# Kernel optimization log

Measured on AMD Instinct MI355X. Metric: run time of the kernel, lower is better.

The kernel has to match this reference:

```python
import jax, jax.numpy as jnp
import numpy as np

N = 50000      # nodes
E = 1_600_000  # edges per metapath graph
M = 3          # meta-path patterns
D = 128        # feature dim (in_size == out_size, GraphConv has no weight)
H = 128        # semantic-attention hidden size


def setup_inputs() -> dict:
    key = jax.random.key(0)
    k1, k2, k3, k4 = jax.random.split(key, 4)
    h = jax.random.normal(k1, (N, D), dtype=jnp.float32)
    # edges[m, 0] = src node ids, edges[m, 1] = dst node ids for metapath m
    edges = jax.random.randint(k2, (M, 2, E), 0, N, dtype=jnp.int32)
    W1 = jax.random.normal(k3, (D, H), dtype=jnp.float32) * 0.05
    b1 = jnp.zeros((H,), dtype=jnp.float32)
    W2 = jax.random.normal(k4, (H, 1), dtype=jnp.float32) * 0.05
    return {"h": h, "edges": edges, "W1": W1, "b1": b1, "W2": W2}


def _graph_conv_both(h, src, dst, n):
    """DGL GraphConv(norm='both', weight=None, bias=None):
    out = D_in^{-1/2} * A @ (D_out^{-1/2} * h), zero degrees clamped to 1."""
    ones = jnp.ones_like(src, dtype=h.dtype)
    out_deg = jax.ops.segment_sum(ones, src, num_segments=n)
    in_deg = jax.ops.segment_sum(ones, dst, num_segments=n)
    norm_src = jax.lax.rsqrt(jnp.maximum(out_deg, 1.0))
    norm_dst = jax.lax.rsqrt(jnp.maximum(in_deg, 1.0))
    msg = (h * norm_src[:, None])[src]                  # [E, D] gather
    agg = jax.ops.segment_sum(msg, dst, num_segments=n)  # [N, D] scatter-add
    return agg * norm_dst[:, None]


def reference(h, edges, W1, b1, W2):
    n = h.shape[0]
    m = edges.shape[0]
    # One normalized sparse aggregation per meta-path (fixed small M).
    z = jnp.stack(
        [_graph_conv_both(h, edges[i, 0], edges[i, 1], n) for i in range(m)],
        axis=1,
    )  # [N, M, D]
    # Semantic attention: project -> tanh -> score, mean over nodes, softmax over M.
    w = jnp.mean(jnp.tanh(z @ W1 + b1) @ W2, axis=0)  # [M, 1]
    beta = jax.nn.softmax(w, axis=0)                  # [M, 1]
    return jnp.sum(beta[None, :, :] * z, axis=1)      # [N, D]
```

## Files before the change

### kernel.cpp

```cpp
#include <hip/hip_runtime.h>
#include <cstdint>
#include <cstddef>

typedef unsigned int  uint;
typedef unsigned short ushort;

#define N_NODES 50000
#define N_EDGES 1600000
#define N_META  3
#define DIM     128

#define BKT       256
#define NBKT      196
#define BIN_CHUNK 16384
#define NCHUNK    98
#define CSR_CAP   10240
#define OCH       128
#define EPC       (N_EDGES / OCH)
#define OWORDS    12500
#define PREP_A    (N_META * OCH)
#define W1C_B     4

#define AT_TILE   64
#define AT_NBLK   782
#define ZSTR      72

__device__ __forceinline__ uint bf16rne(float f) {
    const uint u = __float_as_uint(f);
    return (u + 0x7FFFu + ((u >> 16) & 1u)) >> 16;
}
__device__ __forceinline__ float bflo(uint p) { return __uint_as_float(p << 16); }
__device__ __forceinline__ float bfhi(uint p) { return __uint_as_float(p & 0xFFFF0000u); }
__device__ __forceinline__ float fast_tanh(float x) {
    const float e = __expf(2.0f * x);
    return 1.0f - 2.0f / (e + 1.0f);
}

__global__ __launch_bounds__(256) void prep_kernel(
        const int* __restrict__ edges, const float* __restrict__ W1,
        int* __restrict__ bucket_cnt, uint* __restrict__ partials,
        ushort* __restrict__ W1b) {
    __shared__ __align__(16) uint sh[OWORDS];
    __shared__ uint bh[NBKT];
    const int blk = blockIdx.x;
    if (blk < PREP_A) {
        const int m = blk >> 7, c = blk & 127;
        uint4* sh4 = reinterpret_cast<uint4*>(sh);
        for (int j = threadIdx.x; j < OWORDS / 4; j += 256)
            sh4[j] = make_uint4(0u, 0u, 0u, 0u);
        for (int j = threadIdx.x; j < NBKT; j += 256) bh[j] = 0;
        __syncthreads();
        const int* src = edges + (size_t)(2 * m) * N_EDGES;
        const int* dst = edges + (size_t)(2 * m + 1) * N_EDGES;
        const int beg = c * EPC, end = beg + EPC;
        for (int i = beg + 4 * threadIdx.x; i + 4 <= end; i += 1024) {
            const uint4 s4 = *reinterpret_cast<const uint4*>(src + i);
            const uint4 d4 = *reinterpret_cast<const uint4*>(dst + i);
            atomicAdd(&sh[s4.x >> 2], 1u << (8 * (s4.x & 3)));
            atomicAdd(&sh[s4.y >> 2], 1u << (8 * (s4.y & 3)));
            atomicAdd(&sh[s4.z >> 2], 1u << (8 * (s4.z & 3)));
            atomicAdd(&sh[s4.w >> 2], 1u << (8 * (s4.w & 3)));
            atomicAdd(&bh[d4.x >> 8], 1u);
            atomicAdd(&bh[d4.y >> 8], 1u);
            atomicAdd(&bh[d4.z >> 8], 1u);
            atomicAdd(&bh[d4.w >> 8], 1u);
        }
        __syncthreads();
        uint4* outp4 = reinterpret_cast<uint4*>(
            partials + (size_t)(m * OCH + c) * OWORDS);
        for (int j = threadIdx.x; j < OWORDS / 4; j += 256) outp4[j] = sh4[j];
        for (int j = threadIdx.x; j < NBKT; j += 256)
            if (bh[j]) atomicAdd(&bucket_cnt[m * NBKT + j], (int)bh[j]);
    } else {
        const int base = (blk - PREP_A) * (DIM * DIM / W1C_B);
        for (int i = base + threadIdx.x; i < base + DIM * DIM / W1C_B; i += 256)
            W1b[i] = (ushort)bf16rne(W1[i]);
    }
}

__global__ __launch_bounds__(256) void scan_nsrc_kernel(
        const int* __restrict__ bucket_cnt, int* __restrict__ bucket_off,
        int* __restrict__ bucket_cur, int* __restrict__ row_off,
        const uint* __restrict__ partials, float* __restrict__ nsrc) {
    const int blk = blockIdx.x;
    if (blk < N_META) {
        __shared__ int sc[256];
        const int m = blk, t = threadIdx.x;
        const int v = (t < NBKT) ? bucket_cnt[m * NBKT + t] : 0;
        sc[t] = v;
        __syncthreads();
        for (int off = 1; off < 256; off <<= 1) {
            const int tt = (t >= off) ? sc[t - off] : 0;
            __syncthreads();
            sc[t] += tt;
            __syncthreads();
        }
        const int excl = sc[t] - v;
        if (t < NBKT) {
            bucket_off[m * (NBKT + 1) + t] = excl;
            bucket_cur[m * NBKT + t] = excl;
        }
        if (t == 0) {
            bucket_off[m * (NBKT + 1) + NBKT] = N_EDGES;
            row_off[m * (N_NODES + 1) + N_NODES] = N_EDGES;
        }
    } else {
        const int i = (blk - N_META) * 256 + threadIdx.x;
        if (i < N_META * N_NODES) {
            const int m = i / N_NODES, node = i - m * N_NODES;
            const int q = node >> 2, s8 = 8 * (node & 3);
            int s = 0;
#pragma unroll 8
            for (int c = 0; c < OCH; ++c)
                s += (partials[(size_t)(m * OCH + c) * OWORDS + q] >> s8) & 0xFF;
            nsrc[i] = rsqrtf(fmaxf((float)s, 1.0f));
        }
    }
}

__global__ __launch_bounds__(256) void scale_kernel(
        const float* __restrict__ h, const float* __restrict__ nsrc,
        ushort* __restrict__ hbm) {
    const int i = blockIdx.x * 256 + threadIdx.x;
    const int node = i >> 5;
    const float4 v = reinterpret_cast<const float4*>(h)[i];
    uint2* o = reinterpret_cast<uint2*>(hbm);
#pragma unroll
    for (int m = 0; m < N_META; ++m) {
        const float n = nsrc[m * N_NODES + node];
        uint2 p;
        p.x = bf16rne(v.x * n) | (bf16rne(v.y * n) << 16);
        p.y = bf16rne(v.z * n) | (bf16rne(v.w * n) << 16);
        o[(size_t)m * (N_NODES * DIM / 4) + i] = p;
    }
}

__global__ __launch_bounds__(256) void bin_kernel(
        const int* __restrict__ edges, int* __restrict__ bucket_cur,
        uint* __restrict__ pairs) {
    const int m = blockIdx.y;
    __shared__ int hist[NBKT];
    __shared__ int cur[NBKT];
    for (int j = threadIdx.x; j < NBKT; j += 256) hist[j] = 0;
    __syncthreads();
    const int* src = edges + (size_t)(2 * m) * N_EDGES;
    const int* dst = edges + (size_t)(2 * m + 1) * N_EDGES;
    const int beg = blockIdx.x * BIN_CHUNK;
    const int end = min(beg + BIN_CHUNK, N_EDGES);
    for (int i = beg + 4 * threadIdx.x; i + 4 <= end; i += 1024) {
        const uint4 d4 = *reinterpret_cast<const uint4*>(dst + i);
        atomicAdd(&hist[d4.x >> 8], 1);
        atomicAdd(&hist[d4.y >> 8], 1);
        atomicAdd(&hist[d4.z >> 8], 1);
        atomicAdd(&hist[d4.w >> 8], 1);
    }
    __syncthreads();
    for (int j = threadIdx.x; j < NBKT; j += 256) {
        const int n = hist[j];
        cur[j] = n ? atomicAdd(&bucket_cur[m * NBKT + j], n) : 0;
    }
    __syncthreads();
    uint* pm = pairs + (size_t)m * N_EDGES;
    for (int i = beg + 4 * threadIdx.x; i + 4 <= end; i += 1024) {
        const uint4 s4 = *reinterpret_cast<const uint4*>(src + i);
        const uint4 d4 = *reinterpret_cast<const uint4*>(dst + i);
        int p0 = atomicAdd(&cur[d4.x >> 8], 1);
        pm[p0] = (d4.x << 16) | s4.x;
        int p1 = atomicAdd(&cur[d4.y >> 8], 1);
        pm[p1] = (d4.y << 16) | s4.y;
        int p2 = atomicAdd(&cur[d4.z >> 8], 1);
        pm[p2] = (d4.z << 16) | s4.z;
        int p3 = atomicAdd(&cur[d4.w >> 8], 1);
        pm[p3] = (d4.w << 16) | s4.w;
    }
}

__global__ __launch_bounds__(256) void csr_kernel(
        const uint* __restrict__ pairs, const int* __restrict__ bucket_off,
        int* __restrict__ row_off, ushort* __restrict__ csr) {
    const int b = blockIdx.x, m = blockIdx.y;
    const int node_base = b * BKT;
    const int nb = min(BKT, N_NODES - node_base);
    __shared__ uint stage[CSR_CAP];
    __shared__ int hist[BKT];
    __shared__ int sc[BKT];
    __shared__ int cur[BKT];
    hist[threadIdx.x] = 0;
    __syncthreads();
    const int beg = bucket_off[m * (NBKT + 1) + b];
    const int end = bucket_off[m * (NBKT + 1) + b + 1];
    const int cnt = end - beg;
    const uint* pm = pairs + (size_t)m * N_EDGES + beg;
    for (int i = threadIdx.x; i < cnt; i += 256) {
        const uint p = pm[i];
        if (i < CSR_CAP) stage[i] = p;
        atomicAdd(&hist[(int)(p >> 16) - node_base], 1);
    }
    __syncthreads();
    const int v = hist[threadIdx.x];
    sc[threadIdx.x] = v;
    __syncthreads();
    for (int off = 1; off < BKT; off <<= 1) {
        const int t = (threadIdx.x >= off) ? sc[threadIdx.x - off] : 0;
        __syncthreads();
        sc[threadIdx.x] += t;
        __syncthreads();
    }
    const int excl = sc[threadIdx.x] - v;
    cur[threadIdx.x] = beg + excl;
    if (threadIdx.x < nb)
        row_off[m * (N_NODES + 1) + node_base + threadIdx.x] = beg + excl;
    __syncthreads();
    ushort* cm = csr + (size_t)m * N_EDGES;
    for (int i = threadIdx.x; i < cnt; i += 256) {
        const uint p = (i < CSR_CAP) ? stage[i] : pm[i];
        const int dl = (int)(p >> 16) - node_base;
        const int pos = atomicAdd(&cur[dl], 1);
        cm[pos] = (ushort)(p & 0xFFFFu);
    }
}

__global__ __launch_bounds__(256) void gather_kernel(
        const ushort* __restrict__ hbm, const ushort* __restrict__ csr,
        const int* __restrict__ row_off, ushort* __restrict__ zb) {
    const int m    = blockIdx.y;
    const int wave = threadIdx.x >> 6;
    const int lane = threadIdx.x & 63;
    const int q    = lane >> 4;
    const int c16  = lane & 15;
    const int node = blockIdx.x * 4 + wave;
    const int* ro = row_off + m * (N_NODES + 1);
    const int beg = ro[node];
    const int end = ro[node + 1];
    const ushort* srcs = csr + (size_t)m * N_EDGES;
    const ushort* tab  = hbm + (size_t)m * N_NODES * DIM;
    float acc[8] = {};
    int j = beg;
    for (; j + 16 <= end; j += 16) {
        int s[4]; uint4 hv[4];
#pragma unroll
        for (int u = 0; u < 4; ++u) s[u] = srcs[j + 4 * u + q];
#pragma unroll
        for (int u = 0; u < 4; ++u)
            hv[u] = *reinterpret_cast<const uint4*>(tab + (size_t)s[u] * DIM + c16 * 8);
#pragma unroll
        for (int u = 0; u < 4; ++u) {
            acc[0] += bflo(hv[u].x); acc[1] += bfhi(hv[u].x);
            acc[2] += bflo(hv[u].y); acc[3] += bfhi(hv[u].y);
            acc[4] += bflo(hv[u].z); acc[5] += bfhi(hv[u].z);
            acc[6] += bflo(hv[u].w); acc[7] += bfhi(hv[u].w);
        }
    }
    for (; j + 4 <= end; j += 4) {
        const int s0 = srcs[j + q];
        const uint4 hv = *reinterpret_cast<const uint4*>(tab + (size_t)s0 * DIM + c16 * 8);
        acc[0] += bflo(hv.x); acc[1] += bfhi(hv.x);
        acc[2] += bflo(hv.y); acc[3] += bfhi(hv.y);
        acc[4] += bflo(hv.z); acc[5] += bfhi(hv.z);
        acc[6] += bflo(hv.w); acc[7] += bfhi(hv.w);
    }
    if (j + q < end) {
        const int s0 = srcs[j + q];
        const uint4 hv = *reinterpret_cast<const uint4*>(tab + (size_t)s0 * DIM + c16 * 8);
        acc[0] += bflo(hv.x); acc[1] += bfhi(hv.x);
        acc[2] += bflo(hv.y); acc[3] += bfhi(hv.y);
        acc[4] += bflo(hv.z); acc[5] += bfhi(hv.z);
        acc[6] += bflo(hv.w); acc[7] += bfhi(hv.w);
    }
#pragma unroll
    for (int k = 0; k < 8; ++k) {
        acc[k] += __shfl_xor(acc[k], 16);
        acc[k] += __shfl_xor(acc[k], 32);
    }
    if (lane < 16) {
        const float nd = rsqrtf(fmaxf((float)(end - beg), 1.0f));
        uint4 o;
        o.x = bf16rne(acc[0] * nd) | (bf16rne(acc[1] * nd) << 16);
        o.y = bf16rne(acc[2] * nd) | (bf16rne(acc[3] * nd) << 16);
        o.z = bf16rne(acc[4] * nd) | (bf16rne(acc[5] * nd) << 16);
        o.w = bf16rne(acc[6] * nd) | (bf16rne(acc[7] * nd) << 16);
        *reinterpret_cast<uint4*>(
            zb + ((size_t)m * N_NODES + node) * DIM + c16 * 8) = o;
    }
}

__global__ __launch_bounds__(256) void attn_kernel(
        const ushort* __restrict__ zb, const ushort* __restrict__ W1b,
        const float* __restrict__ b1, const float* __restrict__ W2,
        float* __restrict__ wacc) {
    const int m   = blockIdx.y;
    const int tid = threadIdx.x;
    __shared__ __align__(16) ushort zT[DIM * ZSTR];
    __shared__ __align__(16) ushort w1s[DIM * DIM];
    __shared__ float red[4];

    {
        const uint4* s = reinterpret_cast<const uint4*>(W1b);
        uint4* dst = reinterpret_cast<uint4*>(w1s);
        for (int i = tid; i < DIM * DIM / 8; i += 256) dst[i] = s[i];
    }
    const int node_base = blockIdx.x * AT_TILE;
    for (int i = tid; i < AT_TILE * (DIM / 8); i += 256) {
        const int n = i >> 4, dq = i & 15;
        int row = node_base + n;
        if (row >= N_NODES) row = N_NODES - 1;
        const uint4 v = *reinterpret_cast<const uint4*>(
            zb + ((size_t)m * N_NODES + row) * DIM + dq * 8);
        ushort* cptr = &zT[(8 * dq) * ZSTR + n];
        cptr[0 * ZSTR] = (ushort)(v.x & 0xFFFFu); cptr[1 * ZSTR] = (ushort)(v.x >> 16);
        cptr[2 * ZSTR] = (ushort)(v.y & 0xFFFFu); cptr[3 * ZSTR] = (ushort)(v.y >> 16);
        cptr[4 * ZSTR] = (ushort)(v.z & 0xFFFFu); cptr[5 * ZSTR] = (ushort)(v.z >> 16);
        cptr[6 * ZSTR] = (ushort)(v.w & 0xFFFFu); cptr[7 * ZSTR] = (ushort)(v.w >> 16);
    }
    __syncthreads();

    const int jb = (tid & 31) * 4;
    const int nb = (tid >> 5) * 8;
    float q[8][4] = {};
    for (int d = 0; d < DIM; ++d) {
        const uint4 zp = *reinterpret_cast<const uint4*>(&zT[d * ZSTR + nb]);
        const uint2 wp = *reinterpret_cast<const uint2*>(&w1s[d * DIM + jb]);
        float zv[8];
        zv[0] = bflo(zp.x); zv[1] = bfhi(zp.x);
        zv[2] = bflo(zp.y); zv[3] = bfhi(zp.y);
        zv[4] = bflo(zp.z); zv[5] = bfhi(zp.z);
        zv[6] = bflo(zp.w); zv[7] = bfhi(zp.w);
        float wv[4];
        wv[0] = bflo(wp.x); wv[1] = bfhi(wp.x);
        wv[2] = bflo(wp.y); wv[3] = bfhi(wp.y);
#pragma unroll
        for (int i = 0; i < 8; ++i) {
            q[i][0] = fmaf(zv[i], wv[0], q[i][0]);
            q[i][1] = fmaf(zv[i], wv[1], q[i][1]);
            q[i][2] = fmaf(zv[i], wv[2], q[i][2]);
            q[i][3] = fmaf(zv[i], wv[3], q[i][3]);
        }
    }
    const float4 bv  = *reinterpret_cast<const float4*>(b1 + jb);
    const float4 w2v = *reinterpret_cast<const float4*>(W2 + jb);
    float local = 0.0f;
#pragma unroll
    for (int i = 0; i < 8; ++i) {
        if (node_base + nb + i < N_NODES) {
            local += fast_tanh(q[i][0] + bv.x) * w2v.x;
            local += fast_tanh(q[i][1] + bv.y) * w2v.y;
            local += fast_tanh(q[i][2] + bv.z) * w2v.z;
            local += fast_tanh(q[i][3] + bv.w) * w2v.w;
        }
    }
    for (int off = 32; off > 0; off >>= 1)
        local += __shfl_xor(local, off);
    const int wv_id = tid >> 6;
    if ((tid & 63) == 0) red[wv_id] = local;
    __syncthreads();
    if (tid == 0)
        atomicAdd(&wacc[m], red[0] + red[1] + red[2] + red[3]);
}

__global__ __launch_bounds__(256) void final_kernel(
        const ushort* __restrict__ zb, const float* __restrict__ wacc,
        float* __restrict__ out) {
    const int g = blockIdx.x * 256 + threadIdx.x;
    const float invN = 1.0f / (float)N_NODES;
    const float w0 = wacc[0] * invN, w1 = wacc[1] * invN, w2 = wacc[2] * invN;
    const float mx = fmaxf(w0, fmaxf(w1, w2));
    const float e0 = expf(w0 - mx), e1 = expf(w1 - mx), e2 = expf(w2 - mx);
    const float inv = 1.0f / (e0 + e1 + e2);
    const float beta[3] = {e0 * inv, e1 * inv, e2 * inv};
    float a[8] = {};
#pragma unroll
    for (int m = 0; m < N_META; ++m) {
        const uint4 v = reinterpret_cast<const uint4*>(zb)[
            (size_t)m * (N_NODES * DIM / 8) + g];
        const float bm = beta[m];
        a[0] = fmaf(bflo(v.x), bm, a[0]); a[1] = fmaf(bfhi(v.x), bm, a[1]);
        a[2] = fmaf(bflo(v.y), bm, a[2]); a[3] = fmaf(bfhi(v.y), bm, a[3]);
        a[4] = fmaf(bflo(v.z), bm, a[4]); a[5] = fmaf(bfhi(v.z), bm, a[5]);
        a[6] = fmaf(bflo(v.w), bm, a[6]); a[7] = fmaf(bfhi(v.w), bm, a[7]);
    }
    float4 o0 = {a[0], a[1], a[2], a[3]};
    float4 o1 = {a[4], a[5], a[6], a[7]};
    reinterpret_cast<float4*>(out)[(size_t)g * 2 + 0] = o0;
    reinterpret_cast<float4*>(out)[(size_t)g * 2 + 1] = o1;
}

extern "C" void kernel_launch(void* const* d_in, const int* in_sizes, int n_in,
                              void* d_out, int out_size, void* d_ws, size_t ws_size,
                              hipStream_t stream) {
    const float* h    = (const float*)d_in[0];
    const int*  edges = (const int*)d_in[1];
    const float* W1   = (const float*)d_in[2];
    const float* b1   = (const float*)d_in[3];
    const float* W2   = (const float*)d_in[4];
    float* out = (float*)d_out;

    char* p = (char*)d_ws;
    ushort* zb      = (ushort*)p;
    uint*  pairs    = (uint*)p;
    uint*  partials = (uint*)(p + (size_t)N_META * N_EDGES * 4);
    p += (size_t)N_META * N_NODES * DIM * 2;
    ushort* hbm     = (ushort*)p; p += (size_t)N_META * N_NODES * DIM * 2;
    ushort* csr     = (ushort*)p; p += (size_t)N_META * N_EDGES * 2;
    int* row_off    = (int*)p;    p += ((size_t)N_META * (N_NODES + 1) + 1) * 4;
    float* nsrc     = (float*)p;  p += (size_t)N_META * N_NODES * 4;
    float* wacc     = (float*)p;  p += 16 * 4;
    int* bucket_cnt = (int*)p;    p += (size_t)N_META * NBKT * 4;
    int* bucket_off = (int*)p;    p += (size_t)N_META * (NBKT + 1) * 4 + 4;
    int* bucket_cur = (int*)p;    p += (size_t)N_META * NBKT * 4;
    ushort* W1b     = (ushort*)p; p += (size_t)DIM * DIM * 2;

    hipMemsetAsync(wacc, 0, (16 + (size_t)N_META * NBKT) * 4, stream);

    prep_kernel<<<dim3(PREP_A + W1C_B), 256, 0, stream>>>(
        edges, W1, bucket_cnt, partials, W1b);
    scan_nsrc_kernel<<<dim3(N_META + (N_META * N_NODES + 255) / 256), 256, 0, stream>>>(
        bucket_cnt, bucket_off, bucket_cur, row_off, partials, nsrc);
    scale_kernel<<<dim3(N_NODES * DIM / 4 / 256), 256, 0, stream>>>(h, nsrc, hbm);
    bin_kernel<<<dim3(NCHUNK, N_META), 256, 0, stream>>>(edges, bucket_cur, pairs);
    csr_kernel<<<dim3(NBKT, N_META), 256, 0, stream>>>(pairs, bucket_off, row_off, csr);
    gather_kernel<<<dim3(N_NODES / 4, N_META), 256, 0, stream>>>(
        hbm, csr, row_off, zb);
    attn_kernel<<<dim3(AT_NBLK, N_META), 256, 0, stream>>>(zb, W1b, b1, W2, wacc);
    final_kernel<<<dim3(N_NODES * DIM / 8 / 256), 256, 0, stream>>>(zb, wacc, out);
}
```

Baseline: 435.8 us.

## Use MFMA bf16 matrix cores for semantic-attention projection

Replaces the scalar FMA GEMM in the attention kernel with 16x16x32 bf16 MFMA instructions. Each wave loads its z rows directly into registers instead of transposing them through shared memory. W1 is pre-transposed in the prep kernel and stored in LDS with an XOR swizzle to avoid bank conflicts. This cuts VALU work and LDS traffic for the projection, but it depends on getting the MFMA operand layout right.

```diff
diff --git a/kernel.cpp b/kernel.cpp
--- a/kernel.cpp
+++ b/kernel.cpp
@@ -4,6 +4,8 @@
 
 typedef unsigned int  uint;
 typedef unsigned short ushort;
+typedef short bf16x8 __attribute__((ext_vector_type(8)));
+typedef float f32x4  __attribute__((ext_vector_type(4)));
 
 #define N_NODES 50000
 #define N_EDGES 1600000
@@ -23,7 +25,6 @@
 
 #define AT_TILE   64
 #define AT_NBLK   782
-#define ZSTR      72
 
 __device__ __forceinline__ uint bf16rne(float f) {
     const uint u = __float_as_uint(f);
@@ -39,7 +40,7 @@
 __global__ __launch_bounds__(256) void prep_kernel(
         const int* __restrict__ edges, const float* __restrict__ W1,
         int* __restrict__ bucket_cnt, uint* __restrict__ partials,
-        ushort* __restrict__ W1b) {
+        ushort* __restrict__ W1T) {
     __shared__ __align__(16) uint sh[OWORDS];
     __shared__ uint bh[NBKT];
     const int blk = blockIdx.x;
@@ -73,8 +74,10 @@
             if (bh[j]) atomicAdd(&bucket_cnt[m * NBKT + j], (int)bh[j]);
     } else {
         const int base = (blk - PREP_A) * (DIM * DIM / W1C_B);
-        for (int i = base + threadIdx.x; i < base + DIM * DIM / W1C_B; i += 256)
-            W1b[i] = (ushort)bf16rne(W1[i]);
+        for (int o = base + threadIdx.x; o < base + DIM * DIM / W1C_B; o += 256) {
+            const int j = o >> 7, k = o & 127;
+            W1T[o] = (ushort)bf16rne(W1[k * DIM + j]);
+        }
     }
 }
 
@@ -285,73 +288,73 @@
 }
 
 __global__ __launch_bounds__(256) void attn_kernel(
-        const ushort* __restrict__ zb, const ushort* __restrict__ W1b,
+        const ushort* __restrict__ zb, const ushort* __restrict__ W1T,
         const float* __restrict__ b1, const float* __restrict__ W2,
         float* __restrict__ wacc) {
     const int m   = blockIdx.y;
     const int tid = threadIdx.x;
-    __shared__ __align__(16) ushort zT[DIM * ZSTR];
+    const int wv  = tid >> 6;
+    const int l   = tid & 63;
     __shared__ __align__(16) ushort w1s[DIM * DIM];
     __shared__ float red[4];
 
     {
-        const uint4* s = reinterpret_cast<const uint4*>(W1b);
-        uint4* dst = reinterpret_cast<uint4*>(w1s);
-        for (int i = tid; i < DIM * DIM / 8; i += 256) dst[i] = s[i];
-    }
-    const int node_base = blockIdx.x * AT_TILE;
-    for (int i = tid; i < AT_TILE * (DIM / 8); i += 256) {
-        const int n = i >> 4, dq = i & 15;
-        int row = node_base + n;
-        if (row >= N_NODES) row = N_NODES - 1;
-        const uint4 v = *reinterpret_cast<const uint4*>(
-            zb + ((size_t)m * N_NODES + row) * DIM + dq * 8);
-        ushort* cptr = &zT[(8 * dq) * ZSTR + n];
-        cptr[0 * ZSTR] = (ushort)(v.x & 0xFFFFu); cptr[1 * ZSTR] = (ushort)(v.x >> 16);
-        cptr[2 * ZSTR] = (ushort)(v.y & 0xFFFFu); cptr[3 * ZSTR] = (ushort)(v.y >> 16);
-        cptr[4 * ZSTR] = (ushort)(v.z & 0xFFFFu); cptr[5 * ZSTR] = (ushort)(v.z >> 16);
-        cptr[6 * ZSTR] = (ushort)(v.w & 0xFFFFu); cptr[7 * ZSTR] = (ushort)(v.w >> 16);
-    }
-    __syncthreads();
-
-    const int jb = (tid & 31) * 4;
-    const int nb = (tid >> 5) * 8;
-    float q[8][4] = {};
-    for (int d = 0; d < DIM; ++d) {
-        const uint4 zp = *reinterpret_cast<const uint4*>(&zT[d * ZSTR + nb]);
-        const uint2 wp = *reinterpret_cast<const uint2*>(&w1s[d * DIM + jb]);
-        float zv[8];
-        zv[0] = bflo(zp.x); zv[1] = bfhi(zp.x);
-        zv[2] = bflo(zp.y); zv[3] = bfhi(zp.y);
-        zv[4] = bflo(zp.z); zv[5] = bfhi(zp.z);
-        zv[6] = bflo(zp.w); zv[7] = bfhi(zp.w);
-        float wv[4];
-        wv[0] = bflo(wp.x); wv[1] = bfhi(wp.x);
-        wv[2] = bflo(wp.y); wv[3] = bfhi(wp.y);
-#pragma unroll
-        for (int i = 0; i < 8; ++i) {
-            q[i][0] = fmaf(zv[i], wv[0], q[i][0]);
-            q[i][1] = fmaf(zv[i], wv[1], q[i][1]);
-            q[i][2] = fmaf(zv[i], wv[2], q[i][2]);
-            q[i][3] = fmaf(zv[i], wv[3], q[i][3]);
-        }
-    }
-    const float4 bv  = *reinterpret_cast<const float4*>(b1 + jb);
-    const float4 w2v = *reinterpret_cast<const float4*>(W2 + jb);
+        const uint4* g = reinterpret_cast<const uint4*>(W1T);
+        for (int i = tid; i < DIM * DIM / 8; i += 256) {
+            const int j = i >> 4;
+            const int slot = i ^ (j & 7);
+            *reinterpret_cast<uint4*>(
+                reinterpret_cast<char*>(w1s) + slot * 16) =
+                g[i];
+        }
+    }
+    __syncthreads();
+
+    const int node_base = blockIdx.x * AT_TILE + wv * 16;
+    const int row = l & 15;
+    const int q   = l >> 4;
+    int nload = node_base + row;
+    if (nload >= N_NODES) nload = N_NODES - 1;
+    const ushort* zrow = zb + ((size_t)m * N_NODES + nload) * DIM + q * 8;
+
+    bf16x8 a[4];
+#pragma unroll
+    for (int kk = 0; kk < 4; ++kk)
+        a[kk] = *reinterpret_cast<const bf16x8*>(zrow + kk * 32);
+
+    f32x4 acc[8];
+#pragma unroll
+    for (int ct = 0; ct < 8; ++ct) acc[ct] = (f32x4){0.f, 0.f, 0.f, 0.f};
+
+#pragma unroll
+    for (int kk = 0; kk < 4; ++kk) {
+#pragma unroll
+        for (int ct = 0; ct < 8; ++ct) {
+            const int j = ct * 16 + row;
+            const int slot = (j * 16 + kk * 4 + q) ^ (j & 7);
+            const bf16x8 b = *reinterpret_cast<const bf16x8*>(
+                reinterpret_cast<char*>(w1s) + slot * 16);
+            acc[ct] = __builtin_amdgcn_mfma_f32_16x16x32_bf16(
+                a[kk], b, acc[ct], 0, 0, 0);
+        }
+    }
+
     float local = 0.0f;
 #pragma unroll
-    for (int i = 0; i < 8; ++i) {
-        if (node_base + nb + i < N_NODES) {
-            local += fast_tanh(q[i][0] + bv.x) * w2v.x;
-            local += fast_tanh(q[i][1] + bv.y) * w2v.y;
-            local += fast_tanh(q[i][2] + bv.z) * w2v.z;
-            local += fast_tanh(q[i][3] + bv.w) * w2v.w;
+    for (int ct = 0; ct < 8; ++ct) {
+        const int j = ct * 16 + row;
+        const float b1j = b1[j];
+        const float w2j = W2[j];
+#pragma unroll
+        for (int r = 0; r < 4; ++r) {
+            const int nd = node_base + q * 4 + r;
+            if (nd < N_NODES)
+                local += fast_tanh(acc[ct][r] + b1j) * w2j;
         }
     }
     for (int off = 32; off > 0; off >>= 1)
         local += __shfl_xor(local, off);
-    const int wv_id = tid >> 6;
-    if ((tid & 63) == 0) red[wv_id] = local;
+    if (l == 0) red[wv] = local;
     __syncthreads();
     if (tid == 0)
         atomicAdd(&wacc[m], red[0] + red[1] + red[2] + red[3]);
@@ -407,12 +410,12 @@
     int* bucket_cnt = (int*)p;    p += (size_t)N_META * NBKT * 4;
     int* bucket_off = (int*)p;    p += (size_t)N_META * (NBKT + 1) * 4 + 4;
     int* bucket_cur = (int*)p;    p += (size_t)N_META * NBKT * 4;
-    ushort* W1b     = (ushort*)p; p += (size_t)DIM * DIM * 2;
+    ushort* W1T     = (ushort*)p; p += (size_t)DIM * DIM * 2;
 
     hipMemsetAsync(wacc, 0, (16 + (size_t)N_META * NBKT) * 4, stream);
 
     prep_kernel<<<dim3(PREP_A + W1C_B), 256, 0, stream>>>(
-        edges, W1, bucket_cnt, partials, W1b);
+        edges, W1, bucket_cnt, partials, W1T);
     scan_nsrc_kernel<<<dim3(N_META + (N_META * N_NODES + 255) / 256), 256, 0, stream>>>(
         bucket_cnt, bucket_off, bucket_cur, row_off, partials, nsrc);
     scale_kernel<<<dim3(N_NODES * DIM / 4 / 256), 256, 0, stream>>>(h, nsrc, hbm);
@@ -420,6 +423,6 @@
     csr_kernel<<<dim3(NBKT, N_META), 256, 0, stream>>>(pairs, bucket_off, row_off, csr);
     gather_kernel<<<dim3(N_NODES / 4, N_META), 256, 0, stream>>>(
         hbm, csr, row_off, zb);
-    attn_kernel<<<dim3(AT_NBLK, N_META), 256, 0, stream>>>(zb, W1b, b1, W2, wacc);
+    attn_kernel<<<dim3(AT_NBLK, N_META), 256, 0, stream>>>(zb, W1T, b1, W2, wacc);
     final_kernel<<<dim3(N_NODES * DIM / 8 / 256), 256, 0, stream>>>(zb, wacc, out);
 }
```

Result: faster. 383.0 us (-12.1%).
